# Kernel tuning notes

Measured on AMD Instinct MI355X. Metric: run time of the kernel, lower is better.

Reference implementation:

```python
import jax, jax.numpy as jnp
import numpy as np

B, S, HID = 2, 2048, 4096
H, KV, D = 32, 8, 128
WINDOW = 512
ROPE_THETA = 10000.0


def _rope(x, positions):
    # x: [B, S, h, D]; neox rotate-half over full head_dim
    half = D // 2
    inv_freq = 1.0 / (ROPE_THETA ** (jnp.arange(0, half, dtype=jnp.float32) / half))
    ang = positions.astype(jnp.float32)[..., None] * inv_freq  # [B,S,half]
    cos = jnp.cos(ang)[:, :, None, :]
    sin = jnp.sin(ang)[:, :, None, :]
    x1, x2 = x[..., :half], x[..., half:]
    return jnp.concatenate([x1 * cos - x2 * sin, x2 * cos + x1 * sin], axis=-1)


def _smooth(x, filt):
    # x: [B, S, KV, D]; filt: [2, KV] -> out[t] = prev[t-1]*filt[0] + cur[t]*filt[1]
    prev = jnp.pad(x[:, :-1], ((0, 0), (1, 0), (0, 0), (0, 0)))  # zero at t=0
    return x * filt[1][None, None, :, None] + prev * filt[0][None, None, :, None]


def setup_inputs() -> dict:
    key = jax.random.key(0)
    k1, k2, k3, k4, k5 = jax.random.split(key, 5)
    return {
        "hidden_states": jax.random.normal(k1, (B, S, HID), jnp.float32) * 0.02,
        "positions": jnp.broadcast_to(jnp.arange(S, dtype=jnp.int32), (B, S)),
        "w_pack": jax.random.normal(k2, (HID, (H + 2 * KV) * D), jnp.float32) * (HID ** -0.5),
        "w_o": jax.random.normal(k3, (H * D, HID), jnp.float32) * ((H * D) ** -0.5),
        "conv_k": jax.random.normal(k4, (2, KV), jnp.float32) * 0.5,
        "conv_v": jax.random.normal(k5, (2, KV), jnp.float32) * 0.5,
    }


def reference(hidden_states, positions, w_pack, w_o, conv_k, conv_v):
    qkv = jnp.einsum("bsh,hf->bsf", hidden_states, w_pack)
    q = qkv[..., : H * D].reshape(B, S, H, D)
    k = qkv[..., H * D : (H + KV) * D].reshape(B, S, KV, D)
    v = qkv[..., (H + KV) * D :].reshape(B, S, KV, D)

    # causal depthwise smoothing of k/v (window 2), BEFORE rope
    k = _smooth(k, conv_k)
    v = _smooth(v, conv_v)

    q = _rope(q, positions)
    k = _rope(k, positions)

    g = H // KV  # GQA group size
    k_rep = jnp.repeat(k, g, axis=2)  # [B,S,H,D]
    v_rep = jnp.repeat(v, g, axis=2)

    scale = D ** -0.5
    scores = jnp.einsum("bqhd,bkhd->bhqk", q, k_rep) * scale
    qi = jnp.arange(S)[:, None]
    ki = jnp.arange(S)[None, :]
    mask = (ki <= qi) & (qi - ki < WINDOW)  # causal sliding window
    scores = jnp.where(mask[None, None], scores, jnp.float32(-1e30))
    probs = jax.nn.softmax(scores, axis=-1)
    attn = jnp.einsum("bhqk,bkhd->bqhd", probs, v_rep).reshape(B, S, H * D)
    return jnp.einsum("bsf,fh->bsh", attn, w_o)
```

## Files before the change

kernel.cpp:

```cpp
#include <hip/hip_runtime.h>
#include <stdint.h>

typedef unsigned short u16;
typedef unsigned int   u32;
typedef __bf16 bf16_t;
typedef __attribute__((ext_vector_type(8))) bf16_t bf16x8;
typedef __attribute__((ext_vector_type(4))) float   f32x4;

#define AS_GLOBAL __attribute__((address_space(1)))
#define AS_LDS    __attribute__((address_space(3)))

__device__ __forceinline__ void glds16(const u16* g, u16* l) {
  __builtin_amdgcn_global_load_lds((const AS_GLOBAL u32*)g, (AS_LDS u32*)l, 16, 0, 0);
}
__device__ __forceinline__ u16 f2bf(float f) {
  union { float f; u32 u; } a; a.f = f;
  return (u16)((a.u + 0x7FFFu + ((a.u >> 16) & 1u)) >> 16);
}
__device__ __forceinline__ float bf2f(u16 s) {
  union { u32 u; float f; } a; a.u = ((u32)s) << 16;
  return a.f;
}
union U16x8 { uint4 u; bf16x8 v; };

__global__ __launch_bounds__(256) void cvt_bf16(const float* __restrict__ X, u16* __restrict__ Y) {
  int i = blockIdx.x * 256 + threadIdx.x;
  float4 v = ((const float4*)X)[i];
  ushort4 o; o.x = f2bf(v.x); o.y = f2bf(v.y); o.z = f2bf(v.z); o.w = f2bf(v.w);
  ((ushort4*)Y)[i] = o;
}

__global__ __launch_bounds__(256) void cvt_transpose(const float* __restrict__ W, u16* __restrict__ Wt,
                                                     int K, int N) {
  __shared__ float t[64][65];
  const int n0 = blockIdx.x * 64, k0 = blockIdx.y * 64;
  const int tid = threadIdx.x;
  const int cr = tid >> 4, cc = (tid & 15) * 4;
#pragma unroll
  for (int p = 0; p < 4; ++p) {
    int r = p * 16 + cr;
    float4 v = *(const float4*)&W[(size_t)(k0 + r) * N + n0 + cc];
    t[r][cc] = v.x; t[r][cc + 1] = v.y; t[r][cc + 2] = v.z; t[r][cc + 3] = v.w;
  }
  __syncthreads();
#pragma unroll
  for (int p = 0; p < 4; ++p) {
    int rr = p * 16 + cr;
    ushort4 o;
    o.x = f2bf(t[cc + 0][rr]); o.y = f2bf(t[cc + 1][rr]);
    o.z = f2bf(t[cc + 2][rr]); o.w = f2bf(t[cc + 3][rr]);
    *(ushort4*)&Wt[(size_t)(n0 + rr) * K + k0 + cc] = o;
  }
}

__device__ __forceinline__ void stage256(const u16* gb, u16* ldst, int K, int kc, int tid, int w) {
#pragma unroll
  for (int s = 0; s < 2; ++s) {
    int t = s * 512 + tid;
    int row = t >> 2;
    int slot = (t & 3) ^ ((row >> 1) & 3);
    glds16(gb + (size_t)row * K + kc + slot * 8, ldst + s * 4096 + w * 512);
  }
}
template <int BN>
__device__ __forceinline__ void stageB(const u16* gb, u16* ldst, int K, int k0, int tid, int w) {
  constexpr int NB = BN / 64;
#pragma unroll
  for (int s = 0; s < NB; ++s) {
    int t = s * 512 + tid;
    int rr = t >> 2;
    int kh = rr >= BN ? 1 : 0;
    int row = rr - kh * BN;
    int slot = (t & 3) ^ ((row >> 1) & 3);
    glds16(gb + (size_t)row * K + k0 + kh * 32 + slot * 8, ldst + s * 4096 + w * 512);
  }
}

template <int BN, int WRITE_BF16>
__global__ __launch_bounds__(512, 2) void gemm8p(const u16* __restrict__ A, const u16* __restrict__ Bt,
                                                 void* __restrict__ C, int N, int K) {
  constexpr int NF = BN / 64;
  constexpr int NB = BN / 64;
  constexpr int A_U16 = 2 * 256 * 32;
  constexpr int B_U16 = 2 * BN * 32;
  constexpr int BUF = A_U16 + B_U16;
  __shared__ __align__(16) u16 lds[2 * BUF];

  const int tid = threadIdx.x;
  const int w = tid >> 6, l = tid & 63;
  const int col = l & 15, quad = l >> 4;
  const int m0 = blockIdx.y * 256, n0 = blockIdx.x * BN;
  const int wm = (w >> 2) * 128;
  const int wn = (w & 3) * (BN / 4);

  f32x4 acc[8][NF];
#pragma unroll
  for (int i = 0; i < 8; ++i)
#pragma unroll
    for (int j = 0; j < NF; ++j) acc[i][j] = f32x4{0.f, 0.f, 0.f, 0.f};

  const int sx = ((quad ^ ((col >> 1) & 3)) << 3);
  const int aoff = (wm + col) * 32 + sx;
  const int boff = (wn + col) * 32 + sx;

  const u16* Ab = A + (size_t)m0 * K;
  const u16* Bb = Bt + (size_t)n0 * K;
  const int NT = K >> 6;

  stage256(Ab, &lds[0], K, 0, tid, w);
  stageB<BN>(Bb, &lds[A_U16], K, 0, tid, w);
  stage256(Ab, &lds[8192], K, 32, tid, w);

  for (int t = 0; t < NT; ++t) {
    const int c = t & 1;
    const u16* lA = &lds[c * BUF];
    const u16* lB = &lds[c * BUF + A_U16];
    u16* nA = &lds[(c ^ 1) * BUF];
    u16* nB = &lds[(c ^ 1) * BUF + A_U16];
    const int kn = (t + 1) << 6;
    const bool last = (t == NT - 1);

    bf16x8 a[8], b[NF];
    asm volatile("s_waitcnt vmcnt(2)" ::: "memory");
    __builtin_amdgcn_s_barrier();
    __builtin_amdgcn_sched_barrier(0);
#pragma unroll
    for (int i = 0; i < 8; ++i) a[i] = *(const bf16x8*)&lA[i * 512 + aoff];
    b[0] = *(const bf16x8*)&lB[boff];
    b[1] = *(const bf16x8*)&lB[512 + boff];
    if (!last) stage256(Ab, nA, K, kn, tid, w);
    __builtin_amdgcn_s_setprio(1);
#pragma unroll
    for (int i = 0; i < 8; ++i) {
      acc[i][0] = __builtin_amdgcn_mfma_f32_16x16x32_bf16(a[i], b[0], acc[i][0], 0, 0, 0);
      acc[i][1] = __builtin_amdgcn_mfma_f32_16x16x32_bf16(a[i], b[1], acc[i][1], 0, 0, 0);
    }
    __builtin_amdgcn_s_setprio(0);
#pragma unroll
    for (int j = 2; j < NF; ++j) b[j] = *(const bf16x8*)&lB[j * 512 + boff];
    if (!last) stageB<BN>(Bb, nB, K, kn, tid, w);
    __builtin_amdgcn_s_setprio(1);
#pragma unroll
    for (int i = 0; i < 8; ++i)
#pragma unroll
      for (int j = 2; j < NF; ++j)
        acc[i][j] = __builtin_amdgcn_mfma_f32_16x16x32_bf16(a[i], b[j], acc[i][j], 0, 0, 0);
    __builtin_amdgcn_s_setprio(0);
    if (last) { asm volatile("s_waitcnt vmcnt(0)" ::: "memory"); }
    else if (BN == 256) { asm volatile("s_waitcnt vmcnt(6)" ::: "memory"); }
    else { asm volatile("s_waitcnt vmcnt(5)" ::: "memory"); }
    __builtin_amdgcn_s_barrier();
    __builtin_amdgcn_sched_barrier(0);
#pragma unroll
    for (int i = 0; i < 8; ++i) a[i] = *(const bf16x8*)&lA[8192 + i * 512 + aoff];
    b[0] = *(const bf16x8*)&lB[B_U16 / 2 + boff];
    b[1] = *(const bf16x8*)&lB[B_U16 / 2 + 512 + boff];
    if (!last) stage256(Ab, nA + 8192, K, kn + 32, tid, w);
    __builtin_amdgcn_s_setprio(1);
#pragma unroll
    for (int i = 0; i < 8; ++i) {
      acc[i][0] = __builtin_amdgcn_mfma_f32_16x16x32_bf16(a[i], b[0], acc[i][0], 0, 0, 0);
      acc[i][1] = __builtin_amdgcn_mfma_f32_16x16x32_bf16(a[i], b[1], acc[i][1], 0, 0, 0);
    }
    __builtin_amdgcn_s_setprio(0);
#pragma unroll
    for (int j = 2; j < NF; ++j) b[j] = *(const bf16x8*)&lB[B_U16 / 2 + j * 512 + boff];
    __builtin_amdgcn_s_setprio(1);
#pragma unroll
    for (int i = 0; i < 8; ++i)
#pragma unroll
      for (int j = 2; j < NF; ++j)
        acc[i][j] = __builtin_amdgcn_mfma_f32_16x16x32_bf16(a[i], b[j], acc[i][j], 0, 0, 0);
    __builtin_amdgcn_s_setprio(0);
  }

  if (WRITE_BF16) {
    u16* Cb = (u16*)C;
#pragma unroll
    for (int i = 0; i < 8; ++i)
#pragma unroll
      for (int r = 0; r < 4; ++r) {
        int m = m0 + wm + i * 16 + quad * 4 + r;
        u16* rp = Cb + (size_t)m * N + n0 + wn + col;
#pragma unroll
        for (int j = 0; j < NF; ++j) rp[j * 16] = f2bf(acc[i][j][r]);
      }
  } else {
    float* Cf = (float*)C;
#pragma unroll
    for (int i = 0; i < 8; ++i)
#pragma unroll
      for (int r = 0; r < 4; ++r) {
        int m = m0 + wm + i * 16 + quad * 4 + r;
        float* rp = Cf + (size_t)m * N + n0 + wn + col;
#pragma unroll
        for (int j = 0; j < NF; ++j) rp[j * 16] = acc[i][j][r];
      }
  }
}

__global__ __launch_bounds__(256) void smooth_rope(const u16* __restrict__ QKV, const int* __restrict__ pos,
                                                   const float* __restrict__ ck, const float* __restrict__ cv,
                                                   u16* __restrict__ Q, u16* __restrict__ Kk, u16* __restrict__ V) {
  const int s = blockIdx.x, b = blockIdx.y, tid = threadIdx.x;
  const size_t base = (size_t)(b * 2048 + s) * 6144;
  const bool hasPrev = (s > 0);
  const size_t prev = base - 6144;
  const float p = (float)pos[b * 2048 + s];
  const float L2F = 0.20762050593046f;

  for (int e = tid; e < 2048; e += 256) {
    int h = e >> 6, i = e & 63;
    float x1 = bf2f(QKV[base + h * 128 + i]);
    float x2 = bf2f(QKV[base + h * 128 + 64 + i]);
    float ang = p * exp2f(-(float)i * L2F);
    float sn, cs; __sincosf(ang, &sn, &cs);
    size_t o = ((size_t)(b * 32 + h) * 2048 + s) * 128 + i;
    Q[o] = f2bf(x1 * cs - x2 * sn);
    Q[o + 64] = f2bf(x2 * cs + x1 * sn);
  }
  for (int e = tid; e < 512; e += 256) {
    int kv = e >> 6, i = e & 63;
    size_t off = 4096 + (size_t)kv * 128;
    float f0 = ck[kv], f1 = ck[8 + kv];
    float x1 = bf2f(QKV[base + off + i]) * f1;
    float x2 = bf2f(QKV[base + off + 64 + i]) * f1;
    if (hasPrev) {
      x1 += bf2f(QKV[prev + off + i]) * f0;
      x2 += bf2f(QKV[prev + off + 64 + i]) * f0;
    }
    float ang = p * exp2f(-(float)i * L2F);
    float sn, cs; __sincosf(ang, &sn, &cs);
    size_t o = ((size_t)(b * 8 + kv) * 2048 + s) * 128 + i;
    Kk[o] = f2bf(x1 * cs - x2 * sn);
    Kk[o + 64] = f2bf(x2 * cs + x1 * sn);
  }
  for (int e = tid; e < 1024; e += 256) {
    int kv = e >> 7, d = e & 127;
    size_t off = 5120 + (size_t)kv * 128 + d;
    float f0 = cv[kv], f1 = cv[8 + kv];
    float x = bf2f(QKV[base + off]) * f1;
    if (hasPrev) x += bf2f(QKV[prev + off]) * f0;
    V[((size_t)(b * 8 + kv) * 2048 + s) * 128 + d] = f2bf(x);
  }
}

__global__ __launch_bounds__(256) void transpose_v(const u16* __restrict__ V, u16* __restrict__ Vt) {
  __shared__ u16 t[64][72];
  const int s0 = blockIdx.x * 64, d0 = blockIdx.y * 64, bkv = blockIdx.z;
  const u16* src = V + (size_t)bkv * 2048 * 128;
  u16* dst = Vt + (size_t)bkv * 128 * 2048;
  const int tid = threadIdx.x;
  for (int e = tid; e < 4096; e += 256) {
    int r = e >> 6, c = e & 63;
    t[r][c] = src[(size_t)(s0 + r) * 128 + d0 + c];
  }
  __syncthreads();
  for (int e = tid; e < 4096; e += 256) {
    int r = e >> 6, c = e & 63;
    dst[(size_t)(d0 + r) * 2048 + s0 + c] = t[c][r];
  }
}

__global__ __launch_bounds__(256) void attn_fwd(const u16* __restrict__ Q, const u16* __restrict__ Kk,
                                                const u16* __restrict__ Vt, u16* __restrict__ O) {
  __shared__ union {
    struct { u16 k[64 * 136]; u16 v[128 * 72]; u16 p[4][16 * 72]; } s;
    u16 epi[64 * 136];
  } sm;
  const int tid = threadIdx.x, w = tid >> 6, l = tid & 63;
  const int col = l & 15, quad = l >> 4;
  const int q0 = blockIdx.x * 64;
  const int bh = blockIdx.y;
  const int b = bh >> 5, h = bh & 31, kv = h >> 2;
  const int qrow = q0 + w * 16 + col;
  const int qlo = q0 + w * 16;

  bf16x8 qf[4];
  {
    const u16* qp = Q + ((size_t)((b * 32 + h) * 2048 + qrow)) * 128 + quad * 8;
#pragma unroll
    for (int dc = 0; dc < 4; ++dc) { U16x8 u; u.u = *(const uint4*)(qp + dc * 32); qf[dc] = u.v; }
  }
  const u16* Kbase = Kk + (size_t)(b * 8 + kv) * 2048 * 128;
  const u16* Vbase = Vt + (size_t)(b * 8 + kv) * 128 * 2048;

  f32x4 of[8];
#pragma unroll
  for (int i = 0; i < 8; ++i) of[i] = f32x4{0.f, 0.f, 0.f, 0.f};
  float m_i = -3.0e38f, l_i = 0.f;

  const int s_lo = q0 >= 511 ? q0 - 511 : 0;
  const int kt_lo = s_lo >> 6, kt_hi = q0 >> 6;

  for (int kt = kt_lo; kt <= kt_hi; ++kt) {
    const int k0 = kt * 64;
    __syncthreads();
    for (int sg = tid; sg < 1024; sg += 256) {
      int kr = sg >> 4, kc = sg & 15;
      uint4 kd = *(const uint4*)(Kbase + (size_t)(k0 + kr) * 128 + kc * 8);
      *(uint4*)&sm.s.k[kr * 136 + kc * 8] = kd;
      int vr = sg >> 3, vc = sg & 7;
      uint4 vd = *(const uint4*)(Vbase + (size_t)vr * 2048 + k0 + vc * 8);
      *(uint4*)&sm.s.v[vr * 72 + vc * 8] = vd;
    }
    __syncthreads();

    f32x4 st[4];
#pragma unroll
    for (int t = 0; t < 4; ++t) {
      st[t] = f32x4{0.f, 0.f, 0.f, 0.f};
#pragma unroll
      for (int dc = 0; dc < 4; ++dc) {
        bf16x8 a = *(const bf16x8*)&sm.s.k[(t * 16 + col) * 136 + dc * 32 + quad * 8];
        st[t] = __builtin_amdgcn_mfma_f32_16x16x32_bf16(a, qf[dc], st[t], 0, 0, 0);
      }
    }
    const bool full = (k0 + 63 <= qlo) && (qlo + 15 - k0 < 512);
    float pmax = -3.0e38f;
#pragma unroll
    for (int t = 0; t < 4; ++t)
#pragma unroll
      for (int r = 0; r < 4; ++r) {
        float v = st[t][r] * 0.08838834764831845f;
        if (!full) {
          int key = k0 + t * 16 + quad * 4 + r;
          if (key > qrow || qrow - key >= 512) v = -1.0e30f;
        }
        st[t][r] = v;
        pmax = fmaxf(pmax, v);
      }
    pmax = fmaxf(pmax, __shfl_xor(pmax, 16, 64));
    pmax = fmaxf(pmax, __shfl_xor(pmax, 32, 64));
    float m_new = fmaxf(m_i, pmax);
    float alpha = __expf(m_i - m_new);
    float rsum = 0.f;
#pragma unroll
    for (int t = 0; t < 4; ++t) {
      u16 pk[4];
#pragma unroll
      for (int r = 0; r < 4; ++r) {
        float e = __expf(st[t][r] - m_new);
        rsum += e;
        pk[r] = f2bf(e);
      }
      u32 lo = (u32)pk[0] | ((u32)pk[1] << 16);
      u32 hi = (u32)pk[2] | ((u32)pk[3] << 16);
      *(uint2*)&sm.s.p[w][col * 72 + t * 16 + quad * 4] = make_uint2(lo, hi);
    }
    rsum += __shfl_xor(rsum, 16, 64);
    rsum += __shfl_xor(rsum, 32, 64);
    l_i = l_i * alpha + rsum;
    m_i = m_new;
#pragma unroll
    for (int i = 0; i < 8; ++i) {
      of[i][0] *= alpha; of[i][1] *= alpha; of[i][2] *= alpha; of[i][3] *= alpha;
    }
#pragma unroll
    for (int c = 0; c < 2; ++c) {
      bf16x8 pb = *(const bf16x8*)&sm.s.p[w][col * 72 + c * 32 + quad * 8];
#pragma unroll
      for (int dt = 0; dt < 8; ++dt) {
        bf16x8 a = *(const bf16x8*)&sm.s.v[(dt * 16 + col) * 72 + c * 32 + quad * 8];
        of[dt] = __builtin_amdgcn_mfma_f32_16x16x32_bf16(a, pb, of[dt], 0, 0, 0);
      }
    }
  }
  float invl = 1.f / l_i;
  __syncthreads();
#pragma unroll
  for (int dt = 0; dt < 8; ++dt) {
    u16 pk[4];
#pragma unroll
    for (int r = 0; r < 4; ++r) pk[r] = f2bf(of[dt][r] * invl);
    u32 lo = (u32)pk[0] | ((u32)pk[1] << 16);
    u32 hi = (u32)pk[2] | ((u32)pk[3] << 16);
    *(uint2*)&sm.epi[(w * 16 + col) * 136 + dt * 16 + quad * 4] = make_uint2(lo, hi);
  }
  __syncthreads();
  for (int e = tid; e < 1024; e += 256) {
    int r = e >> 4, c = e & 15;
    uint4 v = *(const uint4*)&sm.epi[r * 136 + c * 8];
    *(uint4*)(O + ((size_t)(b * 2048 + q0 + r) * 4096 + h * 128 + c * 8)) = v;
  }
}

extern "C" void kernel_launch(void* const* d_in, const int* in_sizes, int n_in,
                              void* d_out, int out_size, void* d_ws, size_t ws_size,
                              hipStream_t stream) {
  const float* hs  = (const float*)d_in[0];
  const int*   pos = (const int*)d_in[1];
  const float* wp  = (const float*)d_in[2];
  const float* wo  = (const float*)d_in[3];
  const float* ck  = (const float*)d_in[4];
  const float* cv  = (const float*)d_in[5];
  float* out = (float*)d_out;
  char* ws = (char*)d_ws;

  u16* Xb   = (u16*)(ws);
  u16* Wt   = (u16*)(ws + 33554432);
  u16* QKV  = (u16*)(ws + 83886080);
  u16* Qb   = (u16*)(ws + 134217728);
  u16* Kb   = (u16*)(ws + 167772160);
  u16* Vb   = (u16*)(ws + 176160768);
  u16* Vtb  = (u16*)(ws + 184549376);
  u16* Attn = Xb;
  u16* Wot  = Wt;

  cvt_bf16<<<16384, 256, 0, stream>>>(hs, Xb);
  cvt_transpose<<<dim3(96, 64), 256, 0, stream>>>(wp, Wt, 4096, 6144);
  gemm8p<192, 1><<<dim3(32, 16), 512, 0, stream>>>(Xb, Wt, (void*)QKV, 6144, 4096);
  smooth_rope<<<dim3(2048, 2), 256, 0, stream>>>(QKV, pos, ck, cv, Qb, Kb, Vb);
  transpose_v<<<dim3(32, 2, 16), 256, 0, stream>>>(Vb, Vtb);
  attn_fwd<<<dim3(32, 64), 256, 0, stream>>>(Qb, Kb, Vtb, Attn);
  cvt_transpose<<<dim3(64, 64), 256, 0, stream>>>(wo, Wot, 4096, 4096);
  gemm8p<256, 0><<<dim3(16, 16), 512, 0, stream>>>(Attn, Wot, (void*)out, 4096, 4096);
}
```

Before: 649.4 us.

## Vectorize smooth_rope, drop LDS staging in attention, remap blocks for KV locality

smooth_rope now has each thread handle eight contiguous bf16 values with 16-byte loads and stores instead of scalar element loops. attn_fwd stops staging K and V tiles in shared memory with block-wide barriers and reads MFMA operands straight from global memory (relying on L2 cache). It also remaps block indices so blocks sharing the same KV head run close together. This removes the barriers and the LDS round trip, but each wave now reloads K/V from global or cache, and the direct loads may be less coalesced.

```diff
diff --git a/kernel.cpp b/kernel.cpp
--- a/kernel.cpp
+++ b/kernel.cpp
@@ -21,7 +21,7 @@
   union { u32 u; float f; } a; a.u = ((u32)s) << 16;
   return a.f;
 }
-union U16x8 { uint4 u; bf16x8 v; };
+union U16x8 { uint4 u; bf16x8 v; u16 h[8]; };
 
 __global__ __launch_bounds__(256) void cvt_bf16(const float* __restrict__ X, u16* __restrict__ Y) {
   int i = blockIdx.x * 256 + threadIdx.x;
@@ -80,7 +80,6 @@
 __global__ __launch_bounds__(512, 2) void gemm8p(const u16* __restrict__ A, const u16* __restrict__ Bt,
                                                  void* __restrict__ C, int N, int K) {
   constexpr int NF = BN / 64;
-  constexpr int NB = BN / 64;
   constexpr int A_U16 = 2 * 256 * 32;
   constexpr int B_U16 = 2 * BN * 32;
   constexpr int BUF = A_U16 + B_U16;
@@ -205,43 +204,68 @@
   const int s = blockIdx.x, b = blockIdx.y, tid = threadIdx.x;
   const size_t base = (size_t)(b * 2048 + s) * 6144;
   const bool hasPrev = (s > 0);
-  const size_t prev = base - 6144;
   const float p = (float)pos[b * 2048 + s];
   const float L2F = 0.20762050593046f;
 
-  for (int e = tid; e < 2048; e += 256) {
-    int h = e >> 6, i = e & 63;
-    float x1 = bf2f(QKV[base + h * 128 + i]);
-    float x2 = bf2f(QKV[base + h * 128 + 64 + i]);
-    float ang = p * exp2f(-(float)i * L2F);
-    float sn, cs; __sincosf(ang, &sn, &cs);
-    size_t o = ((size_t)(b * 32 + h) * 2048 + s) * 128 + i;
-    Q[o] = f2bf(x1 * cs - x2 * sn);
-    Q[o + 64] = f2bf(x2 * cs + x1 * sn);
-  }
-  for (int e = tid; e < 512; e += 256) {
-    int kv = e >> 6, i = e & 63;
-    size_t off = 4096 + (size_t)kv * 128;
-    float f0 = ck[kv], f1 = ck[8 + kv];
-    float x1 = bf2f(QKV[base + off + i]) * f1;
-    float x2 = bf2f(QKV[base + off + 64 + i]) * f1;
+  {
+    const int h = tid >> 3, oc = tid & 7;
+    U16x8 a, c;
+    a.u = *(const uint4*)&QKV[base + h * 128 + oc * 8];
+    c.u = *(const uint4*)&QKV[base + h * 128 + 64 + oc * 8];
+    U16x8 o1, o2;
+#pragma unroll
+    for (int j = 0; j < 8; ++j) {
+      int i = oc * 8 + j;
+      float x1 = bf2f(a.h[j]), x2 = bf2f(c.h[j]);
+      float ang = p * exp2f(-(float)i * L2F);
+      float sn, cs; __sincosf(ang, &sn, &cs);
+      o1.h[j] = f2bf(x1 * cs - x2 * sn);
+      o2.h[j] = f2bf(x2 * cs + x1 * sn);
+    }
+    size_t o = ((size_t)(b * 32 + h) * 2048 + s) * 128 + oc * 8;
+    *(uint4*)&Q[o] = o1.u;
+    *(uint4*)&Q[o + 64] = o2.u;
+  }
+  if (tid < 64) {
+    const int kv = tid >> 3, oc = tid & 7;
+    const size_t off = base + 4096 + kv * 128 + oc * 8;
+    const float f0 = ck[kv], f1 = ck[8 + kv];
+    U16x8 a, c;
+    a.u = *(const uint4*)&QKV[off];
+    c.u = *(const uint4*)&QKV[off + 64];
+    U16x8 pa, pc;
+    pa.u = make_uint4(0, 0, 0, 0); pc.u = make_uint4(0, 0, 0, 0);
     if (hasPrev) {
-      x1 += bf2f(QKV[prev + off + i]) * f0;
-      x2 += bf2f(QKV[prev + off + 64 + i]) * f0;
-    }
-    float ang = p * exp2f(-(float)i * L2F);
-    float sn, cs; __sincosf(ang, &sn, &cs);
-    size_t o = ((size_t)(b * 8 + kv) * 2048 + s) * 128 + i;
-    Kk[o] = f2bf(x1 * cs - x2 * sn);
-    Kk[o + 64] = f2bf(x2 * cs + x1 * sn);
-  }
-  for (int e = tid; e < 1024; e += 256) {
-    int kv = e >> 7, d = e & 127;
-    size_t off = 5120 + (size_t)kv * 128 + d;
-    float f0 = cv[kv], f1 = cv[8 + kv];
-    float x = bf2f(QKV[base + off]) * f1;
-    if (hasPrev) x += bf2f(QKV[prev + off]) * f0;
-    V[((size_t)(b * 8 + kv) * 2048 + s) * 128 + d] = f2bf(x);
+      pa.u = *(const uint4*)&QKV[off - 6144];
+      pc.u = *(const uint4*)&QKV[off - 6144 + 64];
+    }
+    U16x8 o1, o2;
+#pragma unroll
+    for (int j = 0; j < 8; ++j) {
+      int i = oc * 8 + j;
+      float x1 = bf2f(a.h[j]) * f1 + bf2f(pa.h[j]) * f0;
+      float x2 = bf2f(c.h[j]) * f1 + bf2f(pc.h[j]) * f0;
+      float ang = p * exp2f(-(float)i * L2F);
+      float sn, cs; __sincosf(ang, &sn, &cs);
+      o1.h[j] = f2bf(x1 * cs - x2 * sn);
+      o2.h[j] = f2bf(x2 * cs + x1 * sn);
+    }
+    size_t o = ((size_t)(b * 8 + kv) * 2048 + s) * 128 + oc * 8;
+    *(uint4*)&Kk[o] = o1.u;
+    *(uint4*)&Kk[o + 64] = o2.u;
+  } else if (tid < 192) {
+    const int u2 = tid - 64;
+    const int kv = u2 >> 4, oc = u2 & 15;
+    const size_t off = base + 5120 + kv * 128 + oc * 8;
+    const float f0 = cv[kv], f1 = cv[8 + kv];
+    U16x8 a; a.u = *(const uint4*)&QKV[off];
+    U16x8 pa; pa.u = make_uint4(0, 0, 0, 0);
+    if (hasPrev) pa.u = *(const uint4*)&QKV[off - 6144];
+    U16x8 o1;
+#pragma unroll
+    for (int j = 0; j < 8; ++j)
+      o1.h[j] = f2bf(bf2f(a.h[j]) * f1 + bf2f(pa.h[j]) * f0);
+    *(uint4*)&V[((size_t)(b * 8 + kv) * 2048 + s) * 128 + oc * 8] = o1.u;
   }
 }
 
@@ -265,13 +289,15 @@
 __global__ __launch_bounds__(256) void attn_fwd(const u16* __restrict__ Q, const u16* __restrict__ Kk,
                                                 const u16* __restrict__ Vt, u16* __restrict__ O) {
   __shared__ union {
-    struct { u16 k[64 * 136]; u16 v[128 * 72]; u16 p[4][16 * 72]; } s;
+    u16 p[4][16 * 72];
     u16 epi[64 * 136];
   } sm;
   const int tid = threadIdx.x, w = tid >> 6, l = tid & 63;
   const int col = l & 15, quad = l >> 4;
-  const int q0 = blockIdx.x * 64;
-  const int bh = blockIdx.y;
+  const int orig = blockIdx.x + (blockIdx.y << 5);
+  const int wid = (orig & 7) * 256 + (orig >> 3);
+  const int q0 = (wid & 31) * 64;
+  const int bh = wid >> 5;
   const int b = bh >> 5, h = bh & 31, kv = h >> 2;
   const int qrow = q0 + w * 16 + col;
   const int qlo = q0 + w * 16;
@@ -284,6 +310,8 @@
   }
   const u16* Kbase = Kk + (size_t)(b * 8 + kv) * 2048 * 128;
   const u16* Vbase = Vt + (size_t)(b * 8 + kv) * 128 * 2048;
+  const u16* Kp = Kbase + (size_t)col * 128 + quad * 8;
+  const u16* Vp = Vbase + (size_t)col * 2048 + quad * 8;
 
   f32x4 of[8];
 #pragma unroll
@@ -295,16 +323,8 @@
 
   for (int kt = kt_lo; kt <= kt_hi; ++kt) {
     const int k0 = kt * 64;
-    __syncthreads();
-    for (int sg = tid; sg < 1024; sg += 256) {
-      int kr = sg >> 4, kc = sg & 15;
-      uint4 kd = *(const uint4*)(Kbase + (size_t)(k0 + kr) * 128 + kc * 8);
-      *(uint4*)&sm.s.k[kr * 136 + kc * 8] = kd;
-      int vr = sg >> 3, vc = sg & 7;
-      uint4 vd = *(const uint4*)(Vbase + (size_t)vr * 2048 + k0 + vc * 8);
-      *(uint4*)&sm.s.v[vr * 72 + vc * 8] = vd;
-    }
-    __syncthreads();
+    const u16* kp0 = Kp + (size_t)k0 * 128;
+    const u16* vp0 = Vp + k0;
 
     f32x4 st[4];
 #pragma unroll
@@ -312,8 +332,8 @@
       st[t] = f32x4{0.f, 0.f, 0.f, 0.f};
 #pragma unroll
       for (int dc = 0; dc < 4; ++dc) {
-        bf16x8 a = *(const bf16x8*)&sm.s.k[(t * 16 + col) * 136 + dc * 32 + quad * 8];
-        st[t] = __builtin_amdgcn_mfma_f32_16x16x32_bf16(a, qf[dc], st[t], 0, 0, 0);
+        U16x8 u; u.u = *(const uint4*)(kp0 + t * 2048 + dc * 32);
+        st[t] = __builtin_amdgcn_mfma_f32_16x16x32_bf16(u.v, qf[dc], st[t], 0, 0, 0);
       }
     }
     const bool full = (k0 + 63 <= qlo) && (qlo + 15 - k0 < 512);
@@ -346,7 +366,7 @@
       }
       u32 lo = (u32)pk[0] | ((u32)pk[1] << 16);
       u32 hi = (u32)pk[2] | ((u32)pk[3] << 16);
-      *(uint2*)&sm.s.p[w][col * 72 + t * 16 + quad * 4] = make_uint2(lo, hi);
+      *(uint2*)&sm.p[w][col * 72 + t * 16 + quad * 4] = make_uint2(lo, hi);
     }
     rsum += __shfl_xor(rsum, 16, 64);
     rsum += __shfl_xor(rsum, 32, 64);
@@ -358,11 +378,11 @@
     }
 #pragma unroll
     for (int c = 0; c < 2; ++c) {
-      bf16x8 pb = *(const bf16x8*)&sm.s.p[w][col * 72 + c * 32 + quad * 8];
+      bf16x8 pb = *(const bf16x8*)&sm.p[w][col * 72 + c * 32 + quad * 8];
 #pragma unroll
       for (int dt = 0; dt < 8; ++dt) {
-        bf16x8 a = *(const bf16x8*)&sm.s.v[(dt * 16 + col) * 72 + c * 32 + quad * 8];
-        of[dt] = __builtin_amdgcn_mfma_f32_16x16x32_bf16(a, pb, of[dt], 0, 0, 0);
+        U16x8 a; a.u = *(const uint4*)(vp0 + (size_t)dt * 32768 + c * 32);
+        of[dt] = __builtin_amdgcn_mfma_f32_16x16x32_bf16(a.v, pb, of[dt], 0, 0, 0);
       }
     }
   }
```

Measured after the change: 844.5 us. +30.0%, slower.
